# Optimization experiments

Hardware: AMD Instinct MI355X
Metric: run time of the kernel (lower is better)

The kernel has to match this reference:

```python
import jax, jax.numpy as jnp
import numpy as np

HEAD, DIM, R = 8, 256, 3
RA = (2 * R + 1) ** 2  # 49


def conv2d(x, w, b=None, pad=0, groups=1):
    y = jax.lax.conv_general_dilated(x, w, (1, 1), [(pad, pad), (pad, pad)],
                                     dimension_numbers=('NCHW', 'OIHW', 'NCHW'),
                                     feature_group_count=groups)
    return y if b is None else y + b[None, :, None, None]


def grid_sample(img, grid, mode, padding='zeros'):
    # img [B,C,H,W]; grid [B,Hg,Wg,2] with (x,y) in [-1,1]; align_corners=False.
    B, C, H, W = img.shape
    Hg, Wg = grid.shape[1], grid.shape[2]
    gx = ((grid[..., 0] + 1.0) * W - 1.0) / 2.0
    gy = ((grid[..., 1] + 1.0) * H - 1.0) / 2.0
    if padding == 'border':
        gx = jnp.clip(gx, 0.0, W - 1.0)
        gy = jnp.clip(gy, 0.0, H - 1.0)
    gx = gx.reshape(B, -1)
    gy = gy.reshape(B, -1)

    def gather(iy, ix):
        iyc = jnp.clip(iy, 0, H - 1)
        ixc = jnp.clip(ix, 0, W - 1)
        return jax.vmap(lambda im, a, b: im[:, a, b])(img, iyc, ixc)  # [B,C,N]

    def mask(iy, ix):
        if padding == 'border':
            return jnp.ones(iy.shape, img.dtype)
        return ((ix >= 0) & (ix < W) & (iy >= 0) & (iy < H)).astype(img.dtype)

    if mode == 'nearest':
        ix = jnp.round(gx).astype(jnp.int32)
        iy = jnp.round(gy).astype(jnp.int32)
        out = gather(iy, ix) * mask(iy, ix)[:, None, :]
    else:  # bilinear
        x0f = jnp.floor(gx); y0f = jnp.floor(gy)
        wx = gx - x0f; wy = gy - y0f
        x0 = x0f.astype(jnp.int32); y0 = y0f.astype(jnp.int32)
        out = jnp.zeros((B, C, gx.shape[1]), img.dtype)
        for dx, dy, w in ((0, 0, (1 - wx) * (1 - wy)), (1, 0, wx * (1 - wy)),
                          (0, 1, (1 - wx) * wy), (1, 1, wx * wy)):
            ix = x0 + dx; iy = y0 + dy
            out = out + gather(iy, ix) * (w * mask(iy, ix))[:, None, :]
    return out.reshape(B, C, Hg, Wg)


def mlp2(x, W1, b1, W2, b2):
    return jax.nn.relu(x @ W1.T + b1) @ W2.T + b2


def setup_inputs() -> dict:
    key = jax.random.key(0)
    ks = jax.random.split(key, 32)
    B, H, W, Q = 1, 64, 64, 4096
    f32 = jnp.float32
    rn = lambda k, shp, s=0.02: jax.random.normal(k, shp, f32) * s
    return {
        'inp': jax.random.normal(ks[0], (B, 3, H, W), f32),
        'coord': jax.random.uniform(ks[1], (B, Q, 2), f32, -1.0, 1.0),
        'cell': jnp.full((B, Q, 2), 2.0 / (2 * H), f32),
        'W_enc': rn(ks[2], (64, 3, 3, 3)), 'b_enc': jnp.zeros((64,), f32),
        'W_ch': rn(ks[3], (256, 64, 3, 3)), 'b_ch': jnp.zeros((256,), f32),
        'W_q': rn(ks[4], (256, 256, 3, 3)), 'b_q': jnp.zeros((256,), f32),
        'W_k': rn(ks[5], (256, 256, 3, 3)), 'b_k': jnp.zeros((256,), f32),
        'W_v': rn(ks[6], (256, 256, 3, 3)), 'b_v': jnp.zeros((256,), f32),
        'W_off1': rn(ks[7], (256, 32, 5, 5)), 'b_off1': jnp.zeros((256,), f32),
        'ln_g': jnp.ones((256,), f32), 'ln_b': jnp.zeros((256,), f32),
        'W_off2': rn(ks[8], (98, 256, 1, 1)),
        'Wc1': rn(ks[9], (256, 98)), 'bc1': jnp.zeros((256,), f32),
        'Wc2': rn(ks[10], (49, 256)), 'bc2': jnp.zeros((49,), f32),
        'Wi1': rn(ks[11], (256, 12546)), 'bi1': jnp.zeros((256,), f32),
        'Wi2': rn(ks[12], (3, 256)), 'bi2': jnp.zeros((3,), f32),
        'scale': 2,
    }


def reference(inp, coord, cell, W_enc, b_enc, W_ch, b_ch, W_q, b_q, W_k, b_k,
              W_v, b_v, W_off1, b_off1, ln_g, ln_b, W_off2, Wc1, bc1, Wc2, bc2,
              Wi1, bi1, Wi2, bi2, scale):
    B, _, H, W = inp.shape
    Q = coord.shape[1]
    # gen_feat: encoder stub (conv+relu) -> conv_ch -> q/k/v convs
    feat = conv2d(jax.nn.relu(conv2d(inp, W_enc, b_enc, pad=1)), W_ch, b_ch, pad=1)
    fq = conv2d(feat, W_q, b_q, pad=1)
    fk = conv2d(feat, W_k, b_k, pad=1)
    fv = conv2d(feat, W_v, b_v, pad=1)
    # offset branch: grouped 5x5 conv -> channelwise LN -> GELU -> 1x1 conv (no bias)
    o = conv2d(feat, W_off1, b_off1, pad=2, groups=8)
    oc = o.transpose(0, 2, 3, 1)
    mu = oc.mean(-1, keepdims=True)
    var = ((oc - mu) ** 2).mean(-1, keepdims=True)
    oc = (oc - mu) / jnp.sqrt(var + 1e-5) * ln_g + ln_b
    offsets = conv2d(jax.nn.gelu(oc.transpose(0, 3, 1, 2), approximate=False), W_off2, None, pad=0)  # [B,98,H,W]
    # LR coordinate grid (y,x) at pixel centers in [-1,1]
    ys = -1.0 + 1.0 / H + (2.0 / H) * jnp.arange(H, dtype=inp.dtype)
    xs = -1.0 + 1.0 / W + (2.0 / W) * jnp.arange(W, dtype=inp.dtype)
    coord_lr = jnp.broadcast_to(jnp.stack(jnp.meshgrid(ys, xs, indexing='ij'), 0)[None], (B, 2, H, W))
    sc = coord[:, :, None, :]          # [B,Q,1,2] (y,x)
    g = sc[..., ::-1]                  # (x,y) for grid_sample
    sck = grid_sample(coord_lr, g, 'nearest').transpose(0, 2, 3, 1)  # [B,Q,1,2]
    off = grid_sample(offsets, g, 'nearest').transpose(0, 2, 3, 1).reshape(B, Q, RA, 2)
    off = jnp.tanh(off) * jnp.array([1.0 / (H - 1.0), 1.0 / (W - 1.0)], inp.dtype) * 2.0
    d = jnp.linspace(-R, R, 2 * R + 1).astype(inp.dtype)
    delta = jnp.stack(jnp.meshgrid(d * (2.0 / H), d * (2.0 / W), indexing='ij'), -1).reshape(1, 1, RA, 2)
    sck = sck + delta + off            # [B,Q,49,2] sampling locs (y,x)
    q = grid_sample(fq, g, 'bilinear').transpose(0, 2, 3, 1).reshape(B, Q, HEAD, DIM // HEAD)
    k = grid_sample(fk, sck[..., ::-1], 'nearest').transpose(0, 2, 3, 1).reshape(B, Q, RA, HEAD, DIM // HEAD)
    v = grid_sample(fv, sck[..., ::-1], 'nearest').transpose(0, 2, 3, 1).reshape(B, Q, RA, HEAD, DIM // HEAD)
    attn_val = jnp.einsum('bqhd,bqkhd->bqkh', q, k) / np.sqrt(DIM // HEAD)  # [B,Q,49,8]
    rel = (sc - sck) * jnp.array([H, W], inp.dtype)  # [B,Q,49,2]
    wcoord = mlp2(rel.reshape(B * Q, RA * 2), Wc1, bc1, Wc2, bc2).reshape(B, Q, RA, 1)
    attn = jax.nn.softmax(wcoord + attn_val, axis=2)  # softmax over 49 samples
    feat_in = (v * attn[..., None]).reshape(B, Q, RA * DIM)
    rel_cell = cell * jnp.array([H, W], inp.dtype)
    feat_in = jnp.concatenate([feat_in, rel_cell], -1)  # [B,Q,12546]
    pred = mlp2(feat_in.reshape(B * Q, -1), Wi1, bi1, Wi2, bi2).reshape(B, Q, 3)
    skip = grid_sample(inp, g, 'bilinear', 'border')[:, :, :, 0].transpose(0, 2, 1)
    return pred + skip
```

## Files before the change

kernel.cpp:

```cpp
#include <hip/hip_runtime.h>
#include <hip/hip_bf16.h>


typedef unsigned short u16;
typedef unsigned int u32;
using frag_ab = __attribute__((ext_vector_type(8))) short;
using frag_cd = __attribute__((ext_vector_type(4))) float;

#define HW 4096
#define NQ 4096
#define KBIG 12576
#define SPLITK 16
#define KCHUNK 800
#define KQ 2304
#define QSPLIT 3
#define QCHUNK 768

static __device__ __forceinline__ u16 f2b(float f) {
  union { __hip_bfloat16 h; u16 u; } c; c.h = __float2bfloat16(f); return c.u;
}
static __device__ __forceinline__ float b2f(u16 v) {
  return __uint_as_float((u32)v << 16);
}
static __device__ __forceinline__ u32 pk2(float a, float b) {
  union { __hip_bfloat162 h; u32 u; } c;
  c.h = __float22bfloat162_rn(float2{a, b});
  return c.u;
}
static __device__ __forceinline__ void glds16(const u16* g, u16* l) {
  __builtin_amdgcn_global_load_lds(
      (const __attribute__((address_space(1))) u32*)(g),
      (__attribute__((address_space(3))) u32*)(l), 16, 0, 0);
}

#define BM 64
#define BN 64
#define BK 32
#define LDSS 40

__global__ __launch_bounds__(256)
void gemm_bt(const u16* __restrict__ A, const u16* __restrict__ Bt,
             void* __restrict__ Cv, const float* __restrict__ bias,
             int N, int K, int ldc, int flags,
             long sA, long sB, long sC, int sBias)
{
  __shared__ u16 As[BM * LDSS];
  __shared__ u16 Bs[BN * LDSS];
  const int z = blockIdx.z;
  A  += (long)z * sA;
  Bt += (long)z * sB;
  const float* bz = bias ? bias + (long)z * sBias : nullptr;

  const int tid  = threadIdx.x;
  const int m0   = blockIdx.x * BM;
  const int n0   = blockIdx.y * BN;
  const int wave = tid >> 6, lane = tid & 63;
  const int mw = (wave & 1) * 32, nw = (wave >> 1) * 32;
  const int lr = lane & 15, lk = lane >> 4;
  const int srow = tid >> 2, scol = (tid & 3) * 8;

  frag_cd acc[2][2] = {};
  const u16* aptr = A + (size_t)(m0 + srow) * K + scol;
  const bool bok  = (n0 + srow) < N;
  const u16* bptr = Bt + (size_t)(n0 + srow) * K + scol;

  uint4 av = *(const uint4*)(aptr);
  uint4 bv = bok ? *(const uint4*)(bptr) : uint4{0u, 0u, 0u, 0u};

  for (int k0 = 0; k0 < K; k0 += BK) {
    *(uint4*)&As[srow * LDSS + scol] = av;
    *(uint4*)&Bs[srow * LDSS + scol] = bv;
    __syncthreads();
    if (k0 + BK < K) {
      av = *(const uint4*)(aptr + k0 + BK);
      bv = bok ? *(const uint4*)(bptr + k0 + BK) : uint4{0u, 0u, 0u, 0u};
    }
    frag_ab af0 = *(const frag_ab*)&As[(mw      + lr) * LDSS + lk * 8];
    frag_ab af1 = *(const frag_ab*)&As[(mw + 16 + lr) * LDSS + lk * 8];
    frag_ab bf0 = *(const frag_ab*)&Bs[(nw      + lr) * LDSS + lk * 8];
    frag_ab bf1 = *(const frag_ab*)&Bs[(nw + 16 + lr) * LDSS + lk * 8];
    acc[0][0] = __builtin_amdgcn_mfma_f32_16x16x32_bf16(af0, bf0, acc[0][0], 0, 0, 0);
    acc[0][1] = __builtin_amdgcn_mfma_f32_16x16x32_bf16(af0, bf1, acc[0][1], 0, 0, 0);
    acc[1][0] = __builtin_amdgcn_mfma_f32_16x16x32_bf16(af1, bf0, acc[1][0], 0, 0, 0);
    acc[1][1] = __builtin_amdgcn_mfma_f32_16x16x32_bf16(af1, bf1, acc[1][1], 0, 0, 0);
    __syncthreads();
  }

  const bool relu = flags & 1;
  const bool obf  = flags & 2;
  #pragma unroll
  for (int i = 0; i < 2; i++)
    #pragma unroll
    for (int j = 0; j < 2; j++) {
      int col = n0 + nw + j * 16 + lr;
      if (col >= N) continue;
      float badd = bz ? bz[col] : 0.f;
      #pragma unroll
      for (int r = 0; r < 4; r++) {
        int row = m0 + mw + i * 16 + lk * 4 + r;
        float v = acc[i][j][r] + badd;
        if (relu) v = fmaxf(v, 0.f);
        size_t idx = (size_t)z * sC + (size_t)row * ldc + col;
        if (obf) ((u16*)Cv)[idx] = f2b(v);
        else     ((float*)Cv)[idx] = v;
      }
    }
}

template<int W3, int SH, int PAD>
__global__ __launch_bounds__(256)
void gemm_conv(const u16* __restrict__ feat, const u16* __restrict__ Bt,
               void* __restrict__ Cv, const float* __restrict__ bias,
               int N, int K, int ldc, int flags, int FC, int cbStride,
               long sB, long sC, int sBias)
{
  __shared__ u16 As[BM * LDSS];
  __shared__ u16 Bs[BN * LDSS];
  const int z = blockIdx.z;
  Bt += (long)z * sB;
  const float* bz = bias ? bias + (long)z * sBias : nullptr;
  const int cb = z * cbStride;

  const int tid  = threadIdx.x;
  const int m0   = blockIdx.x * BM;
  const int n0   = blockIdx.y * BN;
  const int wave = tid >> 6, lane = tid & 63;
  const int mw = (wave & 1) * 32, nw = (wave >> 1) * 32;
  const int lr = lane & 15, lk = lane >> 4;
  const int srow = tid >> 2, scol = (tid & 3) * 8;
  const int p = m0 + srow, y = p >> 6, x = p & 63;

  frag_cd acc[2][2] = {};
  const bool bok  = (n0 + srow) < N;
  const u16* bptr = Bt + (size_t)(n0 + srow) * K + scol;

  auto stageA = [&](int k0) -> uint4 {
    int k = k0 + scol;
    int s = k >> SH;
    int c = k & ((1 << SH) - 1);
    int dy = s / W3, dx = s - dy * W3;
    int yy = y + dy - PAD, xx = x + dx - PAD;
    if (((unsigned)yy < 64u) && ((unsigned)xx < 64u))
      return *(const uint4*)&feat[(size_t)(yy * 64 + xx) * FC + cb + c];
    return uint4{0u, 0u, 0u, 0u};
  };

  uint4 av = stageA(0);
  uint4 bv = bok ? *(const uint4*)(bptr) : uint4{0u, 0u, 0u, 0u};

  for (int k0 = 0; k0 < K; k0 += BK) {
    *(uint4*)&As[srow * LDSS + scol] = av;
    *(uint4*)&Bs[srow * LDSS + scol] = bv;
    __syncthreads();
    if (k0 + BK < K) {
      av = stageA(k0 + BK);
      bv = bok ? *(const uint4*)(bptr + k0 + BK) : uint4{0u, 0u, 0u, 0u};
    }
    frag_ab af0 = *(const frag_ab*)&As[(mw      + lr) * LDSS + lk * 8];
    frag_ab af1 = *(const frag_ab*)&As[(mw + 16 + lr) * LDSS + lk * 8];
    frag_ab bf0 = *(const frag_ab*)&Bs[(nw      + lr) * LDSS + lk * 8];
    frag_ab bf1 = *(const frag_ab*)&Bs[(nw + 16 + lr) * LDSS + lk * 8];
    acc[0][0] = __builtin_amdgcn_mfma_f32_16x16x32_bf16(af0, bf0, acc[0][0], 0, 0, 0);
    acc[0][1] = __builtin_amdgcn_mfma_f32_16x16x32_bf16(af0, bf1, acc[0][1], 0, 0, 0);
    acc[1][0] = __builtin_amdgcn_mfma_f32_16x16x32_bf16(af1, bf0, acc[1][0], 0, 0, 0);
    acc[1][1] = __builtin_amdgcn_mfma_f32_16x16x32_bf16(af1, bf1, acc[1][1], 0, 0, 0);
    __syncthreads();
  }

  const bool relu = flags & 1;
  const bool obf  = flags & 2;
  #pragma unroll
  for (int i = 0; i < 2; i++)
    #pragma unroll
    for (int j = 0; j < 2; j++) {
      int col = n0 + nw + j * 16 + lr;
      if (col >= N) continue;
      float badd = bz ? bz[col] : 0.f;
      #pragma unroll
      for (int r = 0; r < 4; r++) {
        int row = m0 + mw + i * 16 + lk * 4 + r;
        float v = acc[i][j][r] + badd;
        if (relu) v = fmaxf(v, 0.f);
        size_t idx = (size_t)z * sC + (size_t)row * ldc + col;
        if (obf) ((u16*)Cv)[idx] = f2b(v);
        else     ((float*)Cv)[idx] = v;
      }
    }
}

__global__ __launch_bounds__(256)
void gemm_qkv(const u16* __restrict__ feat, const u16* __restrict__ Bt,
              u16* __restrict__ P)
{
  __shared__ u16 As[64 * LDSS];
  __shared__ u16 Bs[128 * 32];
  const int tid  = threadIdx.x;
  const int m0   = blockIdx.x * 64;
  const int n0   = blockIdx.y * 128;
  const int z    = blockIdx.z;
  const int kbeg = z * QCHUNK;
  const int kend = kbeg + QCHUNK;
  const int wave = tid >> 6, lane = tid & 63;
  const int nw = wave * 32;
  const int lr = lane & 15, lk = lane >> 4;
  const int arow = tid >> 2, acol = (tid & 3) * 8;
  const int p = m0 + arow, y = p >> 6, x = p & 63;

  frag_cd acc[4][2] = {};
  const u16* bbase = Bt + (size_t)(n0 + (tid >> 2)) * KQ + (tid & 3) * 8 + kbeg;
  u16* bdst = &Bs[(size_t)tid * 8];

  auto stageA = [&](int k0) -> uint4 {
    int k = k0 + acol;
    int s = k >> 8, c = k & 255;
    int dy = s / 3, dx = s - dy * 3;
    int yy = y + dy - 1, xx = x + dx - 1;
    if (((unsigned)yy < 64u) && ((unsigned)xx < 64u))
      return *(const uint4*)&feat[(size_t)(yy * 64 + xx) * 256 + c];
    return uint4{0u, 0u, 0u, 0u};
  };

  uint4 av = stageA(kbeg);

  for (int k0 = kbeg; k0 < kend; k0 += BK) {
    glds16(bbase + (k0 - kbeg), bdst);
    glds16(bbase + (k0 - kbeg) + (size_t)64 * KQ, bdst + 2048);
    *(uint4*)&As[arow * LDSS + acol] = av;
    __syncthreads();
    if (k0 + BK < kend) av = stageA(k0 + BK);
    frag_ab af[4];
    #pragma unroll
    for (int i = 0; i < 4; i++)
      af[i] = *(const frag_ab*)&As[(i * 16 + lr) * LDSS + lk * 8];
    #pragma unroll
    for (int j = 0; j < 2; j++) {
      frag_ab bf = *(const frag_ab*)&Bs[(nw + j * 16 + lr) * 32 + lk * 8];
      #pragma unroll
      for (int i = 0; i < 4; i++)
        acc[i][j] = __builtin_amdgcn_mfma_f32_16x16x32_bf16(af[i], bf, acc[i][j], 0, 0, 0);
    }
    __syncthreads();
  }

  #pragma unroll
  for (int i = 0; i < 4; i++)
    #pragma unroll
    for (int j = 0; j < 2; j++) {
      int col = n0 + nw + j * 16 + lr;
      #pragma unroll
      for (int r = 0; r < 4; r++) {
        int row = m0 + i * 16 + lk * 4 + r;
        P[(size_t)z * (NQ * 768) + (size_t)row * 768 + col] = f2b(acc[i][j][r]);
      }
    }
}

__global__ __launch_bounds__(256)
void reduce_qkv(const u16* __restrict__ P, const float* __restrict__ bias,
                u16* __restrict__ outb, float* __restrict__ outV)
{
  int i8 = blockIdx.x * 256 + threadIdx.x;
  if (i8 >= NQ * 96) return;
  size_t i = (size_t)i8 * 8;
  int row = (int)(i / 768);
  int c = (int)(i % 768);
  float v[8];
  #pragma unroll
  for (int t = 0; t < 8; t++) v[t] = bias[c + t];
  for (int z = 0; z < QSPLIT; z++) {
    uint4 a = *(const uint4*)&P[(size_t)z * (NQ * 768) + i];
    u32 aw[4] = {a.x, a.y, a.z, a.w};
    #pragma unroll
    for (int t = 0; t < 4; t++) {
      v[2 * t]     += __uint_as_float(aw[t] << 16);
      v[2 * t + 1] += __uint_as_float(aw[t] & 0xffff0000u);
    }
  }
  uint4 ob = {pk2(v[0], v[1]), pk2(v[2], v[3]), pk2(v[4], v[5]), pk2(v[6], v[7])};
  *(uint4*)&outb[i] = ob;
  if (c >= 512) {
    float* dst = outV + (size_t)row * 256 + (c - 512);
    *(float4*)dst       = float4{v[0], v[1], v[2], v[3]};
    *(float4*)(dst + 4) = float4{v[4], v[5], v[6], v[7]};
  }
}

__global__ __launch_bounds__(512, 4)
void gemm_big(const u16* __restrict__ Bt, const float* __restrict__ fqkvV,
              const float* __restrict__ attnval, const int* __restrict__ vidx,
              const float* __restrict__ cell, u16* __restrict__ P)
{
  __shared__ u16 As[128 * LDSS];
  __shared__ u16 Bs[256 * 32];
  __shared__ int   s_vidx[5 * 128];
  __shared__ float s_attn[5 * 128 * 8];
  const int tid  = threadIdx.x;
  const int m0   = blockIdx.x * 128;
  const int z    = blockIdx.y;
  const int kbeg = z * KCHUNK;
  const int kend = min(KBIG, kbeg + KCHUNK);
  const int jbeg = kbeg >> 8;
  const int jcnt = ((kend - 1) >> 8) - jbeg + 1;
  const int wave = tid >> 6, lane = tid & 63;
  const int mw = (wave & 1) * 64, nwv = (wave >> 1) * 64;
  const int lr = lane & 15, lk = lane >> 4;
  const int arow = tid >> 2, acol = (tid & 3) * 8;
  const int q = m0 + arow;

  for (int t = tid; t < 128 * jcnt; t += 512) {
    int r = t & 127, jj = t >> 7;
    int j = jbeg + jj;
    s_vidx[t] = (j < 49) ? vidx[(m0 + r) * 49 + j] : -1;
  }
  for (int t = tid; t < 128 * 8 * jcnt; t += 512) {
    int h = t & 7, rr = (t >> 3) & 127, jj = t >> 10;
    int j = jbeg + jj;
    s_attn[t] = (j < 49) ? attnval[((size_t)((m0 + rr) * 49 + j)) * 8 + h] : 0.f;
  }
  __syncthreads();

  auto loadA = [&](int k0, float4& f0, float4& f1, float& w) {
    const int k = k0 + acol;
    const int j = k >> 8, c = k & 255;
    f0 = float4{0.f, 0.f, 0.f, 0.f};
    f1 = float4{0.f, 0.f, 0.f, 0.f};
    w = 0.f;
    if (j < 49) {
      const int jj = j - jbeg;
      int id = s_vidx[jj * 128 + arow];
      if (id >= 0) {
        w = s_attn[(jj * 128 + arow) * 8 + (c >> 5)];
        const float* src = fqkvV + (size_t)id * 256 + c;
        f0 = *(const float4*)src;
        f1 = *(const float4*)(src + 4);
      }
    } else if (c == 0) {
      f0.x = cell[q * 2]; f0.y = cell[q * 2 + 1];
      w = 64.f;
    }
  };

  frag_cd acc[4][4] = {};
  float4 f0c, f1c; float wc_;
  loadA(kbeg, f0c, f1c, wc_);
  const u16* bbase = Bt + (size_t)(tid >> 2) * KBIG + (tid & 3) * 8 + kbeg;
  u16* bdst = &Bs[(size_t)tid * 8];

  for (int k0 = kbeg; k0 < kend; k0 += BK) {
    glds16(bbase + (k0 - kbeg), bdst);
    glds16(bbase + (k0 - kbeg) + (size_t)128 * KBIG, bdst + 4096);
    {
      uint4 av;
      av.x = pk2(f0c.x * wc_, f0c.y * wc_);
      av.y = pk2(f0c.z * wc_, f0c.w * wc_);
      av.z = pk2(f1c.x * wc_, f1c.y * wc_);
      av.w = pk2(f1c.z * wc_, f1c.w * wc_);
      *(uint4*)&As[arow * LDSS + acol] = av;
    }
    __syncthreads();
    if (k0 + BK < kend) loadA(k0 + BK, f0c, f1c, wc_);
    frag_ab af[4];
    #pragma unroll
    for (int i = 0; i < 4; i++)
      af[i] = *(const frag_ab*)&As[(mw + i * 16 + lr) * LDSS + lk * 8];
    #pragma unroll
    for (int j = 0; j < 4; j++) {
      frag_ab bf = *(const frag_ab*)&Bs[(nwv + j * 16 + lr) * 32 + lk * 8];
      #pragma unroll
      for (int i = 0; i < 4; i++)
        acc[i][j] = __builtin_amdgcn_mfma_f32_16x16x32_bf16(af[i], bf, acc[i][j], 0, 0, 0);
    }
    __syncthreads();
  }

  #pragma unroll
  for (int i = 0; i < 4; i++)
    #pragma unroll
    for (int j = 0; j < 4; j++) {
      int col = nwv + j * 16 + lr;
      #pragma unroll
      for (int r = 0; r < 4; r++) {
        int row = m0 + mw + i * 16 + lk * 4 + r;
        P[(size_t)z * (NQ * 256) + (size_t)row * 256 + col] = f2b(acc[i][j][r]);
      }
    }
}

__global__ __launch_bounds__(256)
void reduce_final(const u16* __restrict__ Pb, const float* __restrict__ bi1,
                  const float* __restrict__ Wi2, const float* __restrict__ bi2,
                  const float* __restrict__ skipb, float* __restrict__ out)
{
  const int q = blockIdx.x, c = threadIdx.x;
  float s = 0.f;
  #pragma unroll
  for (int z = 0; z < SPLITK; z++)
    s += b2f(Pb[(size_t)z * (NQ * 256) + (size_t)q * 256 + c]);
  s += bi1[c];
  s = fmaxf(s, 0.f);

  __shared__ float part[3][4];
  float p0 = s * Wi2[c], p1 = s * Wi2[256 + c], p2 = s * Wi2[512 + c];
  #pragma unroll
  for (int off = 32; off; off >>= 1) {
    p0 += __shfl_xor(p0, off);
    p1 += __shfl_xor(p1, off);
    p2 += __shfl_xor(p2, off);
  }
  if ((c & 63) == 0) {
    int w = c >> 6;
    part[0][w] = p0; part[1][w] = p1; part[2][w] = p2;
  }
  __syncthreads();
  if (c < 3)
    out[q * 3 + c] = bi2[c] + skipb[q * 3 + c]
                   + part[c][0] + part[c][1] + part[c][2] + part[c][3];
}

__global__ __launch_bounds__(512)
void softmax_k(const float* __restrict__ wc, float* __restrict__ attnval)
{
  const int q = blockIdx.x;
  const int tid = threadIdx.x;
  const int hh = tid >> 6, l = tid & 63;
  float v = (l < 49) ? wc[(size_t)q * 49 + l] + attnval[((size_t)q * 49 + l) * 8 + hh]
                     : -1e30f;
  float m = v;
  #pragma unroll
  for (int off = 32; off; off >>= 1) m = fmaxf(m, __shfl_xor(m, off));
  float e = (l < 49) ? expf(v - m) : 0.f;
  float s = e;
  #pragma unroll
  for (int off = 32; off; off >>= 1) s += __shfl_xor(s, off);
  if (l < 49) attnval[((size_t)q * 49 + l) * 8 + hh] = e / s;
}

static __device__ __forceinline__
void packconv(const float* __restrict__ W, u16* __restrict__ Bt,
              int Cin, int K2, int idx)
{
  int o  = idx / (Cin * K2);
  int r  = idx - o * (Cin * K2);
  int ci = r / K2;
  int s  = r - ci * K2;
  Bt[(size_t)o * (Cin * K2) + s * Cin + ci] = f2b(W[idx]);
}
static __device__ __forceinline__
void packcast(const float* __restrict__ W, u16* __restrict__ Bt,
              int Kin, int Kout, int idx)
{
  int n = idx / Kout, k = idx - n * Kout;
  Bt[idx] = f2b(k < Kin ? W[(size_t)n * Kin + k] : 0.f);
}

#define SZ_CH   147456
#define SZ_QKV  589824
#define SZ_OFF1 204800
#define SZ_OFF2 25088
#define SZ_C1   32768
#define SZ_C2   12544
#define SZ_WI1  3219456
#define SZ_PACK (SZ_CH + 3*SZ_QKV + SZ_OFF1 + SZ_OFF2 + SZ_C1 + SZ_C2 + 768 + SZ_WI1)

__global__ void pack_all(const float* W_ch, const float* W_q, const float* W_k,
                         const float* W_v, const float* W_off1, const float* W_off2,
                         const float* Wc1, const float* Wc2, const float* Wi1,
                         const float* b_q, const float* b_k, const float* b_v,
                         u16* Btch, u16* Btqkv, u16* Btoff1, u16* Btoff2,
                         u16* Btc1, u16* Btc2, u16* Wi1p, float* bqkv)
{
  int i = blockIdx.x * 256 + threadIdx.x;
  if (i < SZ_CH) { packconv(W_ch, Btch, 64, 9, i); return; }
  i -= SZ_CH;
  if (i < SZ_QKV) { packconv(W_q, Btqkv, 256, 9, i); return; }
  i -= SZ_QKV;
  if (i < SZ_QKV) { packconv(W_k, Btqkv + (size_t)256 * 2304, 256, 9, i); return; }
  i -= SZ_QKV;
  if (i < SZ_QKV) { packconv(W_v, Btqkv + (size_t)512 * 2304, 256, 9, i); return; }
  i -= SZ_QKV;
  if (i < SZ_OFF1) { packconv(W_off1, Btoff1, 32, 25, i); return; }
  i -= SZ_OFF1;
  if (i < SZ_OFF2) { packcast(W_off2, Btoff2, 256, 256, i); return; }
  i -= SZ_OFF2;
  if (i < SZ_C1) { packcast(Wc1, Btc1, 98, 128, i); return; }
  i -= SZ_C1;
  if (i < SZ_C2) { packcast(Wc2, Btc2, 256, 256, i); return; }
  i -= SZ_C2;
  if (i < 768) {
    bqkv[i] = (i < 256) ? b_q[i] : (i < 512) ? b_k[i - 256] : b_v[i - 512];
    return;
  }
  i -= 768;
  if (i < SZ_WI1) { packcast(Wi1, Wi1p, 12546, 12576, i); }
}

__global__ __launch_bounds__(64)
void conv_enc(const float* __restrict__ inp, const float* __restrict__ W,
              const float* __restrict__ b, u16* __restrict__ feat1)
{
  const int p = blockIdx.x, c = threadIdx.x;
  const int y = p >> 6, x = p & 63;
  float s = b[c];
  #pragma unroll
  for (int ci = 0; ci < 3; ci++)
    #pragma unroll
    for (int dy = 0; dy < 3; dy++) {
      int yy = y + dy - 1;
      if ((unsigned)yy >= 64u) continue;
      #pragma unroll
      for (int dx = 0; dx < 3; dx++) {
        int xx = x + dx - 1;
        if ((unsigned)xx >= 64u) continue;
        s += inp[ci * HW + yy * 64 + xx] * W[((c * 3 + ci) * 3 + dy) * 3 + dx];
      }
    }
  feat1[(size_t)p * 64 + c] = f2b(fmaxf(s, 0.f));
}

__global__ __launch_bounds__(256)
void ln_gelu(const float* __restrict__ x, const float* __restrict__ g,
             const float* __restrict__ b, u16* __restrict__ y)
{
  const int p = blockIdx.x, c = threadIdx.x;
  __shared__ float r1[4], r2[4];
  float v = x[(size_t)p * 256 + c];
  float s1 = v, s2 = v * v;
  #pragma unroll
  for (int off = 32; off; off >>= 1) {
    s1 += __shfl_xor(s1, off);
    s2 += __shfl_xor(s2, off);
  }
  if ((c & 63) == 0) { r1[c >> 6] = s1; r2[c >> 6] = s2; }
  __syncthreads();
  float t1 = r1[0] + r1[1] + r1[2] + r1[3];
  float t2 = r2[0] + r2[1] + r2[2] + r2[3];
  float mu  = t1 * (1.f / 256.f);
  float var = t2 * (1.f / 256.f) - mu * mu;
  float xn = (v - mu) * rsqrtf(var + 1e-5f) * g[c] + b[c];
  float ge = 0.5f * xn * (1.f + erff(xn * 0.70710678118654752f));
  y[(size_t)p * 256 + c] = f2b(ge);
}

__global__ __launch_bounds__(256)
void sampler(const float* __restrict__ coord, const u16* __restrict__ fqkvb,
             const float* __restrict__ offs, const float* __restrict__ inp,
             float* __restrict__ attnval, u16* __restrict__ relbuf,
             int* __restrict__ vidx, float* __restrict__ skipb)
{
  const int q = blockIdx.x;
  const int tid = threadIdx.x;
  __shared__ float s_off[98];
  __shared__ int s_idx[49];
  __shared__ float s_q[256];

  const float c0 = coord[q * 2], c1 = coord[q * 2 + 1];
  const float gxp = ((c1 + 1.f) * 64.f - 1.f) * 0.5f;
  const float gyp = ((c0 + 1.f) * 64.f - 1.f) * 0.5f;
  const int ixn = (int)rintf(gxp), iyn = (int)rintf(gyp);
  const bool inn = ((unsigned)ixn < 64u) && ((unsigned)iyn < 64u);

  if (tid < 98) {
    float v = inn ? offs[(size_t)(iyn * 64 + ixn) * 98 + tid] : 0.f;
    s_off[tid] = tanhf(v) * (2.f / 63.f);
  }
  __syncthreads();

  const float scky = inn ? (-1.f + (float)(2 * iyn + 1) * (1.f / 64.f)) : 0.f;
  const float sckx = inn ? (-1.f + (float)(2 * ixn + 1) * (1.f / 64.f)) : 0.f;

  if (tid < 49) {
    const int a = tid / 7, bb = tid - a * 7;
    float sy = scky + (float)(a - 3) * (2.f / 64.f) + s_off[2 * tid];
    float sx = sckx + (float)(bb - 3) * (2.f / 64.f) + s_off[2 * tid + 1];
    relbuf[(size_t)q * 128 + 2 * tid]     = f2b((c0 - sy) * 64.f);
    relbuf[(size_t)q * 128 + 2 * tid + 1] = f2b((c1 - sx) * 64.f);
    float gx2 = ((sx + 1.f) * 64.f - 1.f) * 0.5f;
    float gy2 = ((sy + 1.f) * 64.f - 1.f) * 0.5f;
    int ix2 = (int)rintf(gx2), iy2 = (int)rintf(gy2);
    int id = (((unsigned)ix2 < 64u) && ((unsigned)iy2 < 64u)) ? (iy2 * 64 + ix2) : -1;
    s_idx[tid] = id;
    vidx[q * 49 + tid] = id;
  } else if (tid >= 98 && tid < 128) {
    relbuf[(size_t)q * 128 + tid] = 0;
  }

  {
    const float x0f = floorf(gxp), y0f = floorf(gyp);
    const float wx = gxp - x0f, wy = gyp - y0f;
    const int x0 = (int)x0f, y0 = (int)y0f;
    float qc = 0.f;
    #pragma unroll
    for (int t = 0; t < 4; t++) {
      int xi = x0 + (t & 1), yi = y0 + (t >> 1);
      if (((unsigned)xi < 64u) && ((unsigned)yi < 64u)) {
        float w = ((t & 1) ? wx : 1.f - wx) * ((t >> 1) ? wy : 1.f - wy);
        qc += w * b2f(fqkvb[(size_t)(yi * 64 + xi) * 768 + tid]);
      }
    }
    s_q[tid] = qc * 0.17677669529663687f;
  }

  if (tid < 3) {
    float gx = fminf(fmaxf(gxp, 0.f), 63.f);
    float gy = fminf(fmaxf(gyp, 0.f), 63.f);
    float xf = floorf(gx), yf = floorf(gy);
    float wxs = gx - xf, wys = gy - yf;
    int xa = (int)xf, ya = (int)yf;
    int xb = min(xa + 1, 63), yb = min(ya + 1, 63);
    const float* ch = inp + tid * HW;
    float v = (1.f - wxs) * (1.f - wys) * ch[ya * 64 + xa]
            + wxs * (1.f - wys) * ch[ya * 64 + xb]
            + (1.f - wxs) * wys * ch[yb * 64 + xa]
            + wxs * wys * ch[yb * 64 + xb];
    skipb[q * 3 + tid] = v;
  }
  __syncthreads();

  const int wave = tid >> 6, lane = tid & 63;
  const int half = lane >> 5, sub = lane & 31;
  const int ch0 = sub * 8;
  const int h = sub >> 2;
  float qv[8];
  #pragma unroll
  for (int i = 0; i < 8; i++) qv[i] = s_q[ch0 + i];

  for (int it = 0; it < 7; it++) {
    int j = it * 8 + wave * 2 + half;
    if (j >= 49) break;
    int id = s_idx[j];
    float p = 0.f;
    if (id >= 0) {
      uint4 kv = *(const uint4*)&fqkvb[(size_t)id * 768 + 256 + ch0];
      u32 w0 = kv.x, w1 = kv.y, w2 = kv.z, w3 = kv.w;
      p = fmaf(qv[0], __uint_as_float(w0 << 16), p);
      p = fmaf(qv[1], __uint_as_float(w0 & 0xffff0000u), p);
      p = fmaf(qv[2], __uint_as_float(w1 << 16), p);
      p = fmaf(qv[3], __uint_as_float(w1 & 0xffff0000u), p);
      p = fmaf(qv[4], __uint_as_float(w2 << 16), p);
      p = fmaf(qv[5], __uint_as_float(w2 & 0xffff0000u), p);
      p = fmaf(qv[6], __uint_as_float(w3 << 16), p);
      p = fmaf(qv[7], __uint_as_float(w3 & 0xffff0000u), p);
    }
    p += __shfl_down(p, 2, 4);
    p += __shfl_down(p, 1, 4);
    if ((sub & 3) == 0) attnval[((size_t)q * 49 + j) * 8 + h] = p;
  }
}

extern "C" void kernel_launch(void* const* d_in, const int* in_sizes, int n_in,
                              void* d_out, int out_size, void* d_ws, size_t ws_size,
                              hipStream_t stream)
{
  const float* inp    = (const float*)d_in[0];
  const float* coord  = (const float*)d_in[1];
  const float* cell   = (const float*)d_in[2];
  const float* W_enc  = (const float*)d_in[3];
  const float* b_enc  = (const float*)d_in[4];
  const float* W_ch   = (const float*)d_in[5];
  const float* b_ch   = (const float*)d_in[6];
  const float* W_q    = (const float*)d_in[7];
  const float* b_q    = (const float*)d_in[8];
  const float* W_k    = (const float*)d_in[9];
  const float* b_k    = (const float*)d_in[10];
  const float* W_v    = (const float*)d_in[11];
  const float* b_v    = (const float*)d_in[12];
  const float* W_off1 = (const float*)d_in[13];
  const float* b_off1 = (const float*)d_in[14];
  const float* ln_g   = (const float*)d_in[15];
  const float* ln_b   = (const float*)d_in[16];
  const float* W_off2 = (const float*)d_in[17];
  const float* Wc1    = (const float*)d_in[18];
  const float* bc1    = (const float*)d_in[19];
  const float* Wc2    = (const float*)d_in[20];
  const float* bc2    = (const float*)d_in[21];
  const float* Wi1    = (const float*)d_in[22];
  const float* bi1    = (const float*)d_in[23];
  const float* Wi2    = (const float*)d_in[24];
  const float* bi2    = (const float*)d_in[25];

  char* base = (char*)d_ws;
  size_t off = 0;
  auto alloc = [&](size_t bytes) -> char* {
    char* r = base + off;
    off = (off + bytes + 255) & ~(size_t)255;
    return r;
  };

  float* obuf   = (float*)alloc((size_t)HW * 256 * 4);
  u16*   ocg    = (u16*)  alloc((size_t)HW * 256 * 2);
  float* offsb  = (float*)alloc((size_t)HW * 98 * 4);
  u16*   feat1  = (u16*)  alloc((size_t)HW * 64 * 2);
  u16*   feat   = (u16*)  alloc((size_t)HW * 256 * 2);
  u16*   hid1   = (u16*)  alloc((size_t)NQ * 256 * 2);
  float* wcb    = (float*)alloc((size_t)NQ * 49 * 4);
  u16*   relbuf = (u16*)  alloc((size_t)NQ * 128 * 2);
  u16*   Btqkv  = (u16*)  alloc((size_t)768 * 2304 * 2);
  u16*   Btch   = (u16*)  alloc((size_t)256 * 576 * 2);
  u16*   Btoff1 = (u16*)  alloc((size_t)256 * 800 * 2);
  u16*   Btoff2 = (u16*)  alloc((size_t)98 * 256 * 2);
  u16*   Btc1   = (u16*)  alloc((size_t)256 * 128 * 2);
  u16*   Btc2   = (u16*)  alloc((size_t)49 * 256 * 2);
  u16* Pb = (u16*)base;
  u16* Pqb = (u16*)(base + ((size_t)36 << 20));
  {
    size_t need = ((size_t)36 << 20) + (size_t)QSPLIT * NQ * 768 * 2;
    if (off < need) off = (need + 255) & ~(size_t)255;
  }
  u16*   fqkvb   = (u16*)  alloc((size_t)HW * 768 * 2);
  float* fqkvV   = (float*)alloc((size_t)HW * 256 * 4);
  float* attnval = (float*)alloc((size_t)NQ * 49 * 8 * 4);
  int*   vidxb   = (int*)  alloc((size_t)NQ * 49 * 4);
  float* skipb   = (float*)alloc((size_t)NQ * 3 * 4);
  u16*   Wi1p    = (u16*)  alloc((size_t)256 * KBIG * 2);
  float* bqkv    = (float*)alloc(768 * 4);
  (void)ws_size; (void)in_sizes; (void)n_in; (void)out_size;

  pack_all<<<(SZ_PACK + 255) / 256, 256, 0, stream>>>(
      W_ch, W_q, W_k, W_v, W_off1, W_off2, Wc1, Wc2, Wi1, b_q, b_k, b_v,
      Btch, Btqkv, Btoff1, Btoff2, Btc1, Btc2, Wi1p, bqkv);

  conv_enc<<<HW, 64, 0, stream>>>(inp, W_enc, b_enc, feat1);
  gemm_conv<3, 6, 1><<<dim3(64, 4, 1), 256, 0, stream>>>(
      feat1, Btch, feat, b_ch, 256, 576, 256, 2, 64, 0, 0, 0, 0);
  gemm_qkv<<<dim3(64, 6, QSPLIT), 256, 0, stream>>>(feat, Btqkv, Pqb);
  reduce_qkv<<<(NQ * 96 + 255) / 256, 256, 0, stream>>>(Pqb, bqkv, fqkvb, fqkvV);
  gemm_conv<5, 5, 2><<<dim3(64, 1, 8), 256, 0, stream>>>(
      feat, Btoff1, obuf, b_off1, 32, 800, 256, 0, 256, 32,
      (long)32 * 800, 32, 32);
  ln_gelu<<<HW, 256, 0, stream>>>(obuf, ln_g, ln_b, ocg);
  gemm_bt<<<dim3(64, 2, 1), 256, 0, stream>>>(ocg, Btoff2, offsb, nullptr,
      98, 256, 98, 0, 0, 0, 0, 0);

  sampler<<<NQ, 256, 0, stream>>>(coord, fqkvb, offsb, inp,
                                  attnval, relbuf, vidxb, skipb);
  gemm_bt<<<dim3(64, 4, 1), 256, 0, stream>>>(relbuf, Btc1, hid1, bc1,
      256, 128, 256, 3, 0, 0, 0, 0);
  gemm_bt<<<dim3(64, 1, 1), 256, 0, stream>>>(hid1, Btc2, wcb, bc2,
      49, 256, 49, 0, 0, 0, 0, 0);
  softmax_k<<<NQ, 512, 0, stream>>>(wcb, attnval);

  gemm_big<<<dim3(32, SPLITK), 512, 0, stream>>>(
      Wi1p, fqkvV, attnval, vidxb, cell, Pb);
  reduce_final<<<NQ, 256, 0, stream>>>(Pb, bi1, Wi2, bi2, skipb, (float*)d_out);
}
```

Baseline: 290.5 us.

## Merge QKV GEMM and offset conv GEMM into one heterogeneous launch

Folds the qkv 3x3-conv GEMM and the grouped 5x5 offset conv GEMM into a single kernel whose blocks branch on block index to do either job. Both read the same feat tensor and are independent, so the goal is to drop one launch and let the smaller offset-conv blocks fill the CUs that sit idle in the qkv GEMM's tail. The offset branch is a hand-specialized copy of the gemm_conv<5,5,2> path that shares LDS with the qkv branch. This adds code duplication, and the combined kernel's register use is set by the heavier branch.

Measured after the change: 287.8 us. No clear change (-0.9%).

```diff
diff --git a/kernel.cpp b/kernel.cpp
--- a/kernel.cpp
+++ b/kernel.cpp
@@ -15,6 +15,8 @@
 #define KQ 2304
 #define QSPLIT 3
 #define QCHUNK 768
+#define NBLK_QKV (64 * 6 * QSPLIT)
+#define NBLK_OFF1 (64 * 8)
 
 static __device__ __forceinline__ u16 f2b(float f) {
   union { __hip_bfloat16 h; u16 u; } c; c.h = __float2bfloat16(f); return c.u;
@@ -189,70 +191,142 @@
 }
 
 __global__ __launch_bounds__(256)
-void gemm_qkv(const u16* __restrict__ feat, const u16* __restrict__ Bt,
-              u16* __restrict__ P)
-{
-  __shared__ u16 As[64 * LDSS];
-  __shared__ u16 Bs[128 * 32];
-  const int tid  = threadIdx.x;
-  const int m0   = blockIdx.x * 64;
-  const int n0   = blockIdx.y * 128;
-  const int z    = blockIdx.z;
-  const int kbeg = z * QCHUNK;
-  const int kend = kbeg + QCHUNK;
+void gemm_feat(const u16* __restrict__ feat, const u16* __restrict__ Btqkv,
+               u16* __restrict__ Pq, const u16* __restrict__ Btoff1,
+               float* __restrict__ obuf, const float* __restrict__ b_off1)
+{
+  __shared__ u16 smem[6656];
+  const int bid = blockIdx.x;
+  const int tid = threadIdx.x;
   const int wave = tid >> 6, lane = tid & 63;
-  const int nw = wave * 32;
   const int lr = lane & 15, lk = lane >> 4;
-  const int arow = tid >> 2, acol = (tid & 3) * 8;
-  const int p = m0 + arow, y = p >> 6, x = p & 63;
-
-  frag_cd acc[4][2] = {};
-  const u16* bbase = Bt + (size_t)(n0 + (tid >> 2)) * KQ + (tid & 3) * 8 + kbeg;
-  u16* bdst = &Bs[(size_t)tid * 8];
-
-  auto stageA = [&](int k0) -> uint4 {
-    int k = k0 + acol;
-    int s = k >> 8, c = k & 255;
-    int dy = s / 3, dx = s - dy * 3;
-    int yy = y + dy - 1, xx = x + dx - 1;
-    if (((unsigned)yy < 64u) && ((unsigned)xx < 64u))
-      return *(const uint4*)&feat[(size_t)(yy * 64 + xx) * 256 + c];
-    return uint4{0u, 0u, 0u, 0u};
-  };
-
-  uint4 av = stageA(kbeg);
-
-  for (int k0 = kbeg; k0 < kend; k0 += BK) {
-    glds16(bbase + (k0 - kbeg), bdst);
-    glds16(bbase + (k0 - kbeg) + (size_t)64 * KQ, bdst + 2048);
-    *(uint4*)&As[arow * LDSS + acol] = av;
-    __syncthreads();
-    if (k0 + BK < kend) av = stageA(k0 + BK);
-    frag_ab af[4];
-    #pragma unroll
-    for (int i = 0; i < 4; i++)
-      af[i] = *(const frag_ab*)&As[(i * 16 + lr) * LDSS + lk * 8];
-    #pragma unroll
-    for (int j = 0; j < 2; j++) {
-      frag_ab bf = *(const frag_ab*)&Bs[(nw + j * 16 + lr) * 32 + lk * 8];
+
+  if (bid < NBLK_QKV) {
+    u16* As = smem;
+    u16* Bs = smem + 64 * 40;
+    const int mz  = bid & 63;
+    const int rest = bid >> 6;
+    const int ny  = rest % 6;
+    const int z   = rest / 6;
+    const int m0  = mz * 64;
+    const int n0  = ny * 128;
+    const int kbeg = z * QCHUNK;
+    const int kend = kbeg + QCHUNK;
+    const int nw = wave * 32;
+    const int arow = tid >> 2, acol = (tid & 3) * 8;
+    const int p = m0 + arow, y = p >> 6, x = p & 63;
+
+    frag_cd acc[4][2] = {};
+    const u16* bbase = Btqkv + (size_t)(n0 + (tid >> 2)) * KQ + (tid & 3) * 8 + kbeg;
+    u16* bdst = &Bs[(size_t)tid * 8];
+
+    auto stageA = [&](int k0) -> uint4 {
+      int k = k0 + acol;
+      int s = k >> 8, c = k & 255;
+      int dy = s / 3, dx = s - dy * 3;
+      int yy = y + dy - 1, xx = x + dx - 1;
+      if (((unsigned)yy < 64u) && ((unsigned)xx < 64u))
+        return *(const uint4*)&feat[(size_t)(yy * 64 + xx) * 256 + c];
+      return uint4{0u, 0u, 0u, 0u};
+    };
+
+    uint4 av = stageA(kbeg);
+
+    for (int k0 = kbeg; k0 < kend; k0 += BK) {
+      glds16(bbase + (k0 - kbeg), bdst);
+      glds16(bbase + (k0 - kbeg) + (size_t)64 * KQ, bdst + 2048);
+      *(uint4*)&As[arow * LDSS + acol] = av;
+      __syncthreads();
+      if (k0 + BK < kend) av = stageA(k0 + BK);
+      frag_ab af[4];
       #pragma unroll
       for (int i = 0; i < 4; i++)
-        acc[i][j] = __builtin_amdgcn_mfma_f32_16x16x32_bf16(af[i], bf, acc[i][j], 0, 0, 0);
-    }
-    __syncthreads();
-  }
-
-  #pragma unroll
-  for (int i = 0; i < 4; i++)
-    #pragma unroll
-    for (int j = 0; j < 2; j++) {
-      int col = n0 + nw + j * 16 + lr;
+        af[i] = *(const frag_ab*)&As[(i * 16 + lr) * LDSS + lk * 8];
       #pragma unroll
-      for (int r = 0; r < 4; r++) {
-        int row = m0 + i * 16 + lk * 4 + r;
-        P[(size_t)z * (NQ * 768) + (size_t)row * 768 + col] = f2b(acc[i][j][r]);
-      }
-    }
+      for (int j = 0; j < 2; j++) {
+        frag_ab bf = *(const frag_ab*)&Bs[(nw + j * 16 + lr) * 32 + lk * 8];
+        #pragma unroll
+        for (int i = 0; i < 4; i++)
+          acc[i][j] = __builtin_amdgcn_mfma_f32_16x16x32_bf16(af[i], bf, acc[i][j], 0, 0, 0);
+      }
+      __syncthreads();
+    }
+
+    #pragma unroll
+    for (int i = 0; i < 4; i++)
+      #pragma unroll
+      for (int j = 0; j < 2; j++) {
+        int col = n0 + nw + j * 16 + lr;
+        #pragma unroll
+        for (int r = 0; r < 4; r++) {
+          int row = m0 + i * 16 + lk * 4 + r;
+          Pq[(size_t)z * (NQ * 768) + (size_t)row * 768 + col] = f2b(acc[i][j][r]);
+        }
+      }
+  } else {
+    u16* As = smem;
+    u16* Bs = smem + 64 * 40;
+    const int t  = bid - NBLK_QKV;
+    const int m0 = (t & 63) * 64;
+    const int g  = t >> 6;
+    const int cb = g * 32;
+    const u16* Bt = Btoff1 + (size_t)g * 32 * 800;
+    const float* bz = b_off1 + g * 32;
+    const int mw = (wave & 1) * 32, nw = (wave >> 1) * 32;
+    const int srow = tid >> 2, scol = (tid & 3) * 8;
+    const int p = m0 + srow, y = p >> 6, x = p & 63;
+
+    frag_cd acc[2][2] = {};
+    const bool bok  = srow < 32;
+    const u16* bptr = Bt + (size_t)srow * 800 + scol;
+
+    auto stageA = [&](int k0) -> uint4 {
+      int k = k0 + scol;
+      int s = k >> 5;
+      int c = k & 31;
+      int dy = s / 5, dx = s - dy * 5;
+      int yy = y + dy - 2, xx = x + dx - 2;
+      if (((unsigned)yy < 64u) && ((unsigned)xx < 64u))
+        return *(const uint4*)&feat[(size_t)(yy * 64 + xx) * 256 + cb + c];
+      return uint4{0u, 0u, 0u, 0u};
+    };
+
+    uint4 av = stageA(0);
+    uint4 bv = bok ? *(const uint4*)(bptr) : uint4{0u, 0u, 0u, 0u};
+
+    for (int k0 = 0; k0 < 800; k0 += BK) {
+      *(uint4*)&As[srow * LDSS + scol] = av;
+      *(uint4*)&Bs[srow * LDSS + scol] = bv;
+      __syncthreads();
+      if (k0 + BK < 800) {
+        av = stageA(k0 + BK);
+        bv = bok ? *(const uint4*)(bptr + k0 + BK) : uint4{0u, 0u, 0u, 0u};
+      }
+      frag_ab af0 = *(const frag_ab*)&As[(mw      + lr) * LDSS + lk * 8];
+      frag_ab af1 = *(const frag_ab*)&As[(mw + 16 + lr) * LDSS + lk * 8];
+      frag_ab bf0 = *(const frag_ab*)&Bs[(nw      + lr) * LDSS + lk * 8];
+      frag_ab bf1 = *(const frag_ab*)&Bs[(nw + 16 + lr) * LDSS + lk * 8];
+      acc[0][0] = __builtin_amdgcn_mfma_f32_16x16x32_bf16(af0, bf0, acc[0][0], 0, 0, 0);
+      acc[0][1] = __builtin_amdgcn_mfma_f32_16x16x32_bf16(af0, bf1, acc[0][1], 0, 0, 0);
+      acc[1][0] = __builtin_amdgcn_mfma_f32_16x16x32_bf16(af1, bf0, acc[1][0], 0, 0, 0);
+      acc[1][1] = __builtin_amdgcn_mfma_f32_16x16x32_bf16(af1, bf1, acc[1][1], 0, 0, 0);
+      __syncthreads();
+    }
+
+    #pragma unroll
+    for (int i = 0; i < 2; i++)
+      #pragma unroll
+      for (int j = 0; j < 2; j++) {
+        int col = nw + j * 16 + lr;
+        if (col >= 32) continue;
+        float badd = bz[col];
+        #pragma unroll
+        for (int r = 0; r < 4; r++) {
+          int row = m0 + mw + i * 16 + lk * 4 + r;
+          obuf[(size_t)row * 256 + g * 32 + col] = acc[i][j][r] + badd;
+        }
+      }
+  }
 }
 
 __global__ __launch_bounds__(256)
@@ -722,11 +796,9 @@
   conv_enc<<<HW, 64, 0, stream>>>(inp, W_enc, b_enc, feat1);
   gemm_conv<3, 6, 1><<<dim3(64, 4, 1), 256, 0, stream>>>(
       feat1, Btch, feat, b_ch, 256, 576, 256, 2, 64, 0, 0, 0, 0);
-  gemm_qkv<<<dim3(64, 6, QSPLIT), 256, 0, stream>>>(feat, Btqkv, Pqb);
+  gemm_feat<<<NBLK_QKV + NBLK_OFF1, 256, 0, stream>>>(
+      feat, Btqkv, Pqb, Btoff1, obuf, b_off1);
   reduce_qkv<<<(NQ * 96 + 255) / 256, 256, 0, stream>>>(Pqb, bqkv, fqkvb, fqkvV);
-  gemm_conv<5, 5, 2><<<dim3(64, 1, 8), 256, 0, stream>>>(
-      feat, Btoff1, obuf, b_off1, 32, 800, 256, 0, 256, 32,
-      (long)32 * 800, 32, 32);
   ln_gelu<<<HW, 256, 0, stream>>>(obuf, ln_g, ln_b, ocg);
   gemm_bt<<<dim3(64, 2, 1), 256, 0, stream>>>(ocg, Btoff2, offsb, nullptr,
       98, 256, 98, 0, 0, 0, 0, 0);
```
